# Kernel tuning notes

Measured on AMD Instinct MI355X. Metric: run time of the kernel, lower is better.

## Reference

```python
import jax, jax.numpy as jnp
import numpy as np

NUM_HEADS = 8
GROUPS = 32
EPS = 1e-5


def setup_inputs() -> dict:
    key = jax.random.key(0)
    k1, k2, k3 = jax.random.split(key, 3)
    B, C, H, W = 16, 512, 64, 64
    x = jax.random.normal(k1, (B, C, H, W), dtype=jnp.float32)
    scale = C ** -0.5  # keep qkv/proj outputs well-scaled
    return {
        "x": x,
        "norm_w": jnp.ones((C,), jnp.float32),
        "norm_b": jnp.zeros((C,), jnp.float32),
        "qkv_w": jax.random.normal(k2, (3 * C, C), dtype=jnp.float32) * scale,
        "qkv_b": jnp.zeros((3 * C,), jnp.float32),
        "proj_w": jax.random.normal(k3, (C, C), dtype=jnp.float32) * scale,
        "proj_b": jnp.zeros((C,), jnp.float32),
    }


def reference(x, norm_w, norm_b, qkv_w, qkv_b, proj_w, proj_b):
    B, C, H, W = x.shape
    N = H * W
    nh = NUM_HEADS
    hd = C // nh

    # GroupNorm(32, C)
    xg = x.reshape(B, GROUPS, C // GROUPS, N)
    mu = xg.mean(axis=(2, 3), keepdims=True)
    var = xg.var(axis=(2, 3), keepdims=True)
    h = ((xg - mu) * jax.lax.rsqrt(var + EPS)).reshape(B, C, N)
    h = h * norm_w[None, :, None] + norm_b[None, :, None]

    h = h.transpose(0, 2, 1)  # [B, N, C]
    qkv = (h @ qkv_w.T + qkv_b).reshape(B, N, 3, nh, hd)
    q, k, v = qkv[:, :, 0], qkv[:, :, 1], qkv[:, :, 2]  # each [B, N, nh, hd]

    # Faithful to source: attention over the HEAD axis at each position
    attn = jnp.einsum('bnhd,bngd->bnhg', q, k) * (hd ** -0.5)  # [B, N, nh, nh]
    attn = jax.nn.softmax(attn, axis=-1)
    o = jnp.einsum('bnhg,bngd->bnhd', attn, v).reshape(B, N, C)

    o = o @ proj_w.T + proj_b  # [B, N, C]
    return x + o.transpose(0, 2, 1).reshape(B, C, H, W)
```

## Files before the change

kernel.cpp:

```cpp
#include <hip/hip_runtime.h>

typedef __attribute__((ext_vector_type(8))) short short8v;
typedef __attribute__((ext_vector_type(4))) float float4v;
typedef unsigned short ushortT;

__device__ __forceinline__ unsigned short f2bf(float f) {
  union { float f; unsigned u; } a; a.f = f;
  unsigned r = a.u + 0x7fffu + ((a.u >> 16) & 1u);
  return (unsigned short)(r >> 16);
}
__device__ __forceinline__ float2 up2(unsigned u) {
  union { unsigned u; float f; } a, b;
  a.u = u << 16; b.u = u & 0xffff0000u;
  return make_float2(a.f, b.f);
}
__device__ __forceinline__ void gl_lds16(const void* g, void* l) {
  __builtin_amdgcn_global_load_lds(
      (const __attribute__((address_space(1))) void*)g,
      (__attribute__((address_space(3))) void*)l, 16, 0, 0);
}

#define WAITV4 asm volatile("s_waitcnt vmcnt(4)" ::: "memory")
#define WAITV0 asm volatile("s_waitcnt vmcnt(0)" ::: "memory")
#define BAR()  __builtin_amdgcn_s_barrier()
#define MFMA16(d, a, b) d = __builtin_amdgcn_mfma_f32_16x16x32_bf16(a, b, d, 0, 0, 0)

__global__ __launch_bounds__(256) void prep(const float* __restrict__ qkvw,
                                            const float* __restrict__ pw,
                                            const float* __restrict__ x,
                                            ushortT* __restrict__ wq_b,
                                            ushortT* __restrict__ wp_b,
                                            float2* __restrict__ stats) {
  int bid = blockIdx.x, tid = threadIdx.x;
  if (bid < 1024) {
    const float* src = (bid < 768) ? qkvw : pw;
    ushortT* dst     = (bid < 768) ? wq_b : wp_b;
    int base = (bid < 768) ? bid : (bid - 768);
    int i = (base * 256 + tid) * 4;
    float4 v = *(const float4*)(src + i);
    uint2 o;
    o.x = (unsigned)f2bf(v.x) | ((unsigned)f2bf(v.y) << 16);
    o.y = (unsigned)f2bf(v.z) | ((unsigned)f2bf(v.w) << 16);
    *(uint2*)(dst + i) = o;
    return;
  }
  int bg = bid - 1024;
  const float* base = x + (size_t)bg * 65536;
  float s = 0.f, s2 = 0.f;
  for (int i = tid; i < 16384; i += 256) {
    float4 v = *(const float4*)(base + (size_t)i * 4);
    s  += v.x + v.y + v.z + v.w;
    s2 += v.x * v.x + v.y * v.y + v.z * v.z + v.w * v.w;
  }
  #pragma unroll
  for (int off = 32; off > 0; off >>= 1) {
    s  += __shfl_down(s, off);
    s2 += __shfl_down(s2, off);
  }
  __shared__ float red[8];
  int w = tid >> 6, l = tid & 63;
  if (l == 0) { red[w] = s; red[w + 4] = s2; }
  __syncthreads();
  if (tid == 0) {
    float ts = red[0] + red[1] + red[2] + red[3];
    float t2 = red[4] + red[5] + red[6] + red[7];
    float mean = ts * (1.f / 65536.f);
    float var  = t2 * (1.f / 65536.f) - mean * mean;
    stats[bg] = make_float2(mean, rsqrtf(var + 1e-5f));
  }
}

__global__ __launch_bounds__(512) void norm_tr(const float* __restrict__ x,
                                               const float* __restrict__ nw,
                                               const float* __restrict__ nb,
                                               const float2* __restrict__ stats,
                                               ushortT* __restrict__ h) {
  __shared__ float t[64][65];
  int n0 = blockIdx.x * 64, c0 = blockIdx.y * 64, b = blockIdx.z;
  int tx = threadIdx.x, ty = threadIdx.y;
  #pragma unroll
  for (int j = ty; j < 64; j += 8) {
    int c = c0 + j;
    float2 ms = stats[b * 32 + (c >> 4)];
    float v = x[((size_t)b * 512 + c) * 4096 + n0 + tx];
    t[j][tx] = (v - ms.x) * ms.y * nw[c] + nb[c];
  }
  __syncthreads();
  #pragma unroll
  for (int j = ty; j < 64; j += 8) {
    int n = n0 + j;
    h[((size_t)b * 4096 + n) * 512 + c0 + tx] = f2bf(t[tx][j]);
  }
}

__device__ __forceinline__ void core256b(const ushortT* __restrict__ A,
                                         const ushortT* __restrict__ Bm,
                                         ushortT* lds, int m0, int n0,
                                         float4v (&acc)[8][4]) {
  char* ldsb = (char*)lds;
  const int tid = threadIdx.x;
  const int w = tid >> 6, l = tid & 63;
  const int wm = w >> 2, wn = w & 3;

  const int P0b = tid * 16, P1b = 8192 + tid * 16;
  const int r0 = P0b >> 7, r1 = P1b >> 7;
  const int s0 = (P0b & 127) ^ ((r0 & 7) << 4);
  const int s1 = (P1b & 127) ^ ((r1 & 7) << 4);
  const size_t g0 = (size_t)r0 * 512 + (s0 >> 1);
  const size_t g1 = (size_t)r1 * 512 + (s1 >> 1);
  auto stage = [&](const ushortT* mat, int rowbase, int kt, int bufb, int region) {
    const ushortT* gsrc = mat + (size_t)rowbase * 512 + kt * 64;
    char* dbase = ldsb + bufb + region;
    gl_lds16(gsrc + g0, dbase + P0b);
    gl_lds16(gsrc + g1, dbase + P1b);
  };

  const int colb = (l >> 4) * 16;
  const int cs0 = colb ^ ((l & 7) << 4);
  const int cs1 = (64 + colb) ^ ((l & 7) << 4);
  const int arow = wm * 16384 + (l & 15) * 128;
  const int brow = 32768 + wn * 8192 + (l & 15) * 128;

  short8v Af[4][2], Bf[4][2];

  #define RDA4(bb, MH)                                                  \
    { _Pragma("unroll")                                                 \
      for (int mm = 0; mm < 4; ++mm) {                                  \
        const char* p = ldsb + (bb) + arow + ((MH)*4 + mm) * 2048;      \
        Af[mm][0] = *(const short8v*)(p + cs0);                         \
        Af[mm][1] = *(const short8v*)(p + cs1);                         \
      } }
  #define RDB2(bb, N0)                                                  \
    { _Pragma("unroll")                                                 \
      for (int nn = 0; nn < 2; ++nn) {                                  \
        const char* p = ldsb + (bb) + brow + ((N0) + nn) * 2048;        \
        Bf[(N0)+nn][0] = *(const short8v*)(p + cs0);                    \
        Bf[(N0)+nn][1] = *(const short8v*)(p + cs1);                    \
      } }
  #define CLUSTER(MH, NP)                                               \
    { __builtin_amdgcn_s_setprio(1);                                    \
      _Pragma("unroll")                                                 \
      for (int mm = 0; mm < 4; ++mm) {                                  \
        _Pragma("unroll")                                               \
        for (int nn = 0; nn < 2; ++nn) {                                \
          MFMA16(acc[(MH)*4+mm][(NP)*2+nn], Af[mm][0], Bf[(NP)*2+nn][0]); \
          MFMA16(acc[(MH)*4+mm][(NP)*2+nn], Af[mm][1], Bf[(NP)*2+nn][1]); \
        } }                                                             \
      __builtin_amdgcn_s_setprio(0); }

  auto tile = [&](int bb, int t1, int t2, bool s1g, bool s2g, int vw) {
    RDB2(bb, 0); RDA4(bb, 0);
    if (s1g) stage(A, m0 + 128, t1, bb ^ 65536, 16384);
    BAR();
    CLUSTER(0, 0);
    BAR();
    RDB2(bb, 2);
    if (s1g) stage(Bm, n0 + 128, t1, bb ^ 65536, 49152);
    BAR();
    CLUSTER(0, 1);
    BAR();
    RDA4(bb, 1);
    if (s2g) stage(Bm, n0, t2, bb, 32768);
    BAR();
    CLUSTER(1, 1);
    BAR();
    if (s2g) stage(A, m0, t2, bb, 0);
    if (vw == 4)      { WAITV4; }
    else if (vw == 0) { WAITV0; }
    BAR();
    CLUSTER(1, 0);
    BAR();
  };

  stage(A,  m0,       0, 0, 0);
  stage(A,  m0 + 128, 0, 0, 16384);
  stage(Bm, n0,       0, 0, 32768);
  stage(Bm, n0 + 128, 0, 0, 49152);
  stage(Bm, n0,       1, 65536, 32768);
  stage(A,  m0,       1, 65536, 0);
  WAITV4;
  BAR();

  #pragma unroll 1
  for (int tp = 0; tp < 3; ++tp) {
    tile(0,     2 * tp + 1, 2 * tp + 2, true, true, 4);
    tile(65536, 2 * tp + 2, 2 * tp + 3, true, true, 4);
  }
  tile(0,     7, 8, true,  false, 0);
  tile(65536, 8, 9, false, false, -1);
  #undef RDA4
  #undef RDB2
  #undef CLUSTER
}

__global__ __launch_bounds__(512, 2) void gemm_qkv(const ushortT* __restrict__ h,
                                                   const ushortT* __restrict__ wq,
                                                   const float* __restrict__ bias,
                                                   ushortT* __restrict__ outq) {
  __shared__ ushortT lds[65536];
  int bid = blockIdx.x;
  int wg = (bid & 7) * 192 + (bid >> 3);
  int m0 = (wg / 6) * 256, n0 = (wg % 6) * 256;
  float4v acc[8][4] = {};
  core256b(h, wq, lds, m0, n0, acc);
  const int tid = threadIdx.x;
  const int w = tid >> 6, l = tid & 63;
  const int wm = w >> 2, wn = w & 3;
  __syncthreads();
  ushortT* es = lds + w * 1280;
  float bb[4];
  #pragma unroll
  for (int fn = 0; fn < 4; ++fn) bb[fn] = bias[n0 + wn * 64 + fn * 16 + (l & 15)];
  int r = l >> 2, g = l & 3;
  #pragma unroll
  for (int fm = 0; fm < 8; ++fm) {
    #pragma unroll
    for (int fn = 0; fn < 4; ++fn)
      #pragma unroll
      for (int j = 0; j < 4; ++j)
        es[((l >> 4) * 4 + j) * 72 + fn * 16 + (l & 15)] = f2bf(acc[fm][fn][j] + bb[fn]);
    uint4 v0 = *(const uint4*)(es + r * 72 + g * 16);
    uint4 v1 = *(const uint4*)(es + r * 72 + g * 16 + 8);
    size_t mrow = (size_t)m0 + wm * 128 + fm * 16 + r;
    uint4* dst = (uint4*)(outq + mrow * 1536 + n0 + wn * 64 + g * 16);
    dst[0] = v0; dst[1] = v1;
  }
}

__global__ __launch_bounds__(256) void attn_k(const ushortT* __restrict__ qkv,
                                              ushortT* __restrict__ o) {
  int gp = blockIdx.x * 256 + threadIdx.x;
  int pos = gp >> 3, hh = gp & 7;
  const ushortT* base = qkv + (size_t)pos * 1536;

  float lg[8];
  {
    unsigned qu[32];
    const uint4* qs = (const uint4*)(base + hh * 64);
    #pragma unroll
    for (int i = 0; i < 8; ++i) {
      uint4 u = qs[i];
      qu[i*4+0] = u.x; qu[i*4+1] = u.y; qu[i*4+2] = u.z; qu[i*4+3] = u.w;
    }
    #pragma unroll
    for (int g = 0; g < 8; ++g) {
      float s = 0.f;
      #pragma unroll
      for (int d8 = 0; d8 < 8; ++d8) {
        uint4 kk = *(const uint4*)(base + 512 + g * 64 + d8 * 8);
        float2 k0 = up2(kk.x), k1 = up2(kk.y), k2 = up2(kk.z), k3 = up2(kk.w);
        float2 q0 = up2(qu[d8*4+0]), q1 = up2(qu[d8*4+1]);
        float2 q2 = up2(qu[d8*4+2]), q3 = up2(qu[d8*4+3]);
        s += q0.x*k0.x + q0.y*k0.y + q1.x*k1.x + q1.y*k1.y
           + q2.x*k2.x + q2.y*k2.y + q3.x*k3.x + q3.y*k3.y;
      }
      lg[g] = s * 0.125f;
    }
  }
  float mx = lg[0];
  #pragma unroll
  for (int g = 1; g < 8; ++g) mx = fmaxf(mx, lg[g]);
  float ssum = 0.f;
  #pragma unroll
  for (int g = 0; g < 8; ++g) { lg[g] = __expf(lg[g] - mx); ssum += lg[g]; }
  float inv = 1.f / ssum;
  #pragma unroll
  for (int g = 0; g < 8; ++g) lg[g] *= inv;

  ushortT* dst = o + (size_t)pos * 512 + hh * 64;
  #pragma unroll 1
  for (int half = 0; half < 2; ++half) {
    float oa[32];
    #pragma unroll
    for (int i = 0; i < 32; ++i) oa[i] = 0.f;
    const ushortT* vb = base + 1024 + half * 32;
    #pragma unroll
    for (int g = 0; g < 8; ++g) {
      float wg = lg[g];
      #pragma unroll
      for (int d4 = 0; d4 < 4; ++d4) {
        uint4 vv = *(const uint4*)(vb + g * 64 + d4 * 8);
        float2 v0 = up2(vv.x), v1 = up2(vv.y), v2 = up2(vv.z), v3 = up2(vv.w);
        oa[d4*8+0] += wg*v0.x; oa[d4*8+1] += wg*v0.y;
        oa[d4*8+2] += wg*v1.x; oa[d4*8+3] += wg*v1.y;
        oa[d4*8+4] += wg*v2.x; oa[d4*8+5] += wg*v2.y;
        oa[d4*8+6] += wg*v3.x; oa[d4*8+7] += wg*v3.y;
      }
    }
    #pragma unroll
    for (int i = 0; i < 4; ++i) {
      uint4 w_;
      w_.x = (unsigned)f2bf(oa[i*8+0]) | ((unsigned)f2bf(oa[i*8+1]) << 16);
      w_.y = (unsigned)f2bf(oa[i*8+2]) | ((unsigned)f2bf(oa[i*8+3]) << 16);
      w_.z = (unsigned)f2bf(oa[i*8+4]) | ((unsigned)f2bf(oa[i*8+5]) << 16);
      w_.w = (unsigned)f2bf(oa[i*8+6]) | ((unsigned)f2bf(oa[i*8+7]) << 16);
      *(uint4*)(dst + half * 32 + i * 8) = w_;
    }
  }
}

__global__ __launch_bounds__(512, 2) void gemm_proj(const ushortT* __restrict__ o,
                                                    const ushortT* __restrict__ wp,
                                                    const float* __restrict__ bias,
                                                    const float* __restrict__ x,
                                                    float* __restrict__ out) {
  __shared__ ushortT lds[65536];
  int bid = blockIdx.x;
  int wg = (bid & 7) * 64 + (bid >> 3);
  int m0 = (wg >> 1) * 256, n0 = (wg & 1) * 256;
  float4v acc[8][4] = {};
  core256b(o, wp, lds, m0, n0, acc);
  const int tid = threadIdx.x;
  const int w = tid >> 6, l = tid & 63;
  const int wm = w >> 2, wn = w & 3;
  __syncthreads();
  float* es = (float*)((char*)lds + w * 4608);
  int b = m0 >> 12;
  int c = n0 + wn * 64 + l;
  float bc = bias[c];
  const float* xrow = x + ((size_t)b * 512 + c) * 4096;
  float* orow = out + ((size_t)b * 512 + c) * 4096;
  int nb0 = (m0 & 4095) + wm * 128;
  #pragma unroll
  for (int fm = 0; fm < 8; ++fm) {
    #pragma unroll
    for (int fn = 0; fn < 4; ++fn)
      #pragma unroll
      for (int j = 0; j < 4; ++j)
        es[((l >> 4) * 4 + j) * 68 + fn * 16 + (l & 15)] = acc[fm][fn][j];
    int nb = nb0 + fm * 16;
    #pragma unroll
    for (int q4 = 0; q4 < 4; ++q4) {
      float4 xv = *(const float4*)(xrow + nb + q4 * 4);
      float4 ov;
      ov.x = xv.x + bc + es[(q4 * 4 + 0) * 68 + l];
      ov.y = xv.y + bc + es[(q4 * 4 + 1) * 68 + l];
      ov.z = xv.z + bc + es[(q4 * 4 + 2) * 68 + l];
      ov.w = xv.w + bc + es[(q4 * 4 + 3) * 68 + l];
      *(float4*)(orow + nb + q4 * 4) = ov;
    }
  }
}

extern "C" void kernel_launch(void* const* d_in, const int* in_sizes, int n_in,
                              void* d_out, int out_size, void* d_ws, size_t ws_size,
                              hipStream_t stream) {
  const float* x     = (const float*)d_in[0];
  const float* nw    = (const float*)d_in[1];
  const float* nb    = (const float*)d_in[2];
  const float* qkvw  = (const float*)d_in[3];
  const float* qkvb  = (const float*)d_in[4];
  const float* pw    = (const float*)d_in[5];
  const float* pb    = (const float*)d_in[6];
  float* out = (float*)d_out;
  char* ws = (char*)d_ws;

  const size_t OFF_WQ   = 4096;
  const size_t OFF_WP   = OFF_WQ + 1572864;
  const size_t OFF_H    = OFF_WP + 524288;
  const size_t OFF_QKV  = OFF_H + 67108864;

  float2* stats   = (float2*)ws;
  ushortT* wq_b   = (ushortT*)(ws + OFF_WQ);
  ushortT* wp_b   = (ushortT*)(ws + OFF_WP);
  ushortT* h      = (ushortT*)(ws + OFF_H);
  ushortT* qkv    = (ushortT*)(ws + OFF_QKV);

  prep<<<1536, 256, 0, stream>>>(qkvw, pw, x, wq_b, wp_b, stats);
  norm_tr<<<dim3(64, 8, 16), dim3(64, 8), 0, stream>>>(x, nw, nb, stats, h);
  gemm_qkv<<<1536, 512, 0, stream>>>(h, wq_b, qkvb, qkv);
  attn_k<<<2048, 256, 0, stream>>>(qkv, h);
  gemm_proj<<<512, 512, 0, stream>>>(h, wp_b, pb, x, out);
}
```

Measured before the change: 402.6 us.

## Stage per-position QKV rows in LDS and split head dim across thread pairs

The attention kernel now bulk-loads 16 positions' full QKV rows into shared memory with direct global-to-LDS copies, then computes from LDS. Each head's 64-dim work is split across two threads, with the partial dot products combined by a lane shuffle, and the grid size is doubled. This targets the redundant, uncoalesced global reads of K and V (each read by all 8 head threads) and cuts per-thread register pressure, at the cost of a barrier and LDS usage.

```diff
diff --git a/kernel.cpp b/kernel.cpp
--- a/kernel.cpp
+++ b/kernel.cpp
@@ -229,33 +229,47 @@
 
 __global__ __launch_bounds__(256) void attn_k(const ushortT* __restrict__ qkv,
                                               ushortT* __restrict__ o) {
-  int gp = blockIdx.x * 256 + threadIdx.x;
-  int pos = gp >> 3, hh = gp & 7;
-  const ushortT* base = qkv + (size_t)pos * 1536;
-
+  __shared__ ushortT kv[16 * 1544];
+  const int tid = threadIdx.x;
+  const int p0 = blockIdx.x * 16;
+
+  #pragma unroll
+  for (int j = 0; j < 12; ++j) {
+    int c = j * 256 + tid;
+    int row = c / 192, col = c % 192;
+    gl_lds16(qkv + (size_t)(p0 + row) * 1536 + col * 8,
+             (char*)kv + row * 3088 + col * 16);
+  }
+  __syncthreads();
+
+  const int pos = tid >> 4, h = (tid >> 1) & 7, dh = tid & 1;
+  const ushortT* rowp = kv + pos * 1544;
+
+  unsigned qv[16];
+  {
+    const uint4* qs = (const uint4*)(rowp + h * 64 + dh * 32);
+    #pragma unroll
+    for (int i = 0; i < 4; ++i) {
+      uint4 u = qs[i];
+      qv[i*4+0] = u.x; qv[i*4+1] = u.y; qv[i*4+2] = u.z; qv[i*4+3] = u.w;
+    }
+  }
   float lg[8];
-  {
-    unsigned qu[32];
-    const uint4* qs = (const uint4*)(base + hh * 64);
-    #pragma unroll
-    for (int i = 0; i < 8; ++i) {
-      uint4 u = qs[i];
-      qu[i*4+0] = u.x; qu[i*4+1] = u.y; qu[i*4+2] = u.z; qu[i*4+3] = u.w;
+  #pragma unroll
+  for (int g = 0; g < 8; ++g) {
+    const uint4* ks = (const uint4*)(rowp + 512 + g * 64 + dh * 32);
+    float s = 0.f;
+    #pragma unroll
+    for (int i = 0; i < 4; ++i) {
+      uint4 u = ks[i];
+      float2 k0 = up2(u.x), k1 = up2(u.y), k2 = up2(u.z), k3 = up2(u.w);
+      float2 q0 = up2(qv[i*4+0]), q1 = up2(qv[i*4+1]);
+      float2 q2 = up2(qv[i*4+2]), q3 = up2(qv[i*4+3]);
+      s += q0.x*k0.x + q0.y*k0.y + q1.x*k1.x + q1.y*k1.y
+         + q2.x*k2.x + q2.y*k2.y + q3.x*k3.x + q3.y*k3.y;
     }
-    #pragma unroll
-    for (int g = 0; g < 8; ++g) {
-      float s = 0.f;
-      #pragma unroll
-      for (int d8 = 0; d8 < 8; ++d8) {
-        uint4 kk = *(const uint4*)(base + 512 + g * 64 + d8 * 8);
-        float2 k0 = up2(kk.x), k1 = up2(kk.y), k2 = up2(kk.z), k3 = up2(kk.w);
-        float2 q0 = up2(qu[d8*4+0]), q1 = up2(qu[d8*4+1]);
-        float2 q2 = up2(qu[d8*4+2]), q3 = up2(qu[d8*4+3]);
-        s += q0.x*k0.x + q0.y*k0.y + q1.x*k1.x + q1.y*k1.y
-           + q2.x*k2.x + q2.y*k2.y + q3.x*k3.x + q3.y*k3.y;
-      }
-      lg[g] = s * 0.125f;
-    }
+    s += __shfl_xor(s, 1);
+    lg[g] = s * 0.125f;
   }
   float mx = lg[0];
   #pragma unroll
@@ -267,35 +281,32 @@
   #pragma unroll
   for (int g = 0; g < 8; ++g) lg[g] *= inv;
 
-  ushortT* dst = o + (size_t)pos * 512 + hh * 64;
-  #pragma unroll 1
-  for (int half = 0; half < 2; ++half) {
-    float oa[32];
-    #pragma unroll
-    for (int i = 0; i < 32; ++i) oa[i] = 0.f;
-    const ushortT* vb = base + 1024 + half * 32;
-    #pragma unroll
-    for (int g = 0; g < 8; ++g) {
-      float wg = lg[g];
-      #pragma unroll
-      for (int d4 = 0; d4 < 4; ++d4) {
-        uint4 vv = *(const uint4*)(vb + g * 64 + d4 * 8);
-        float2 v0 = up2(vv.x), v1 = up2(vv.y), v2 = up2(vv.z), v3 = up2(vv.w);
-        oa[d4*8+0] += wg*v0.x; oa[d4*8+1] += wg*v0.y;
-        oa[d4*8+2] += wg*v1.x; oa[d4*8+3] += wg*v1.y;
-        oa[d4*8+4] += wg*v2.x; oa[d4*8+5] += wg*v2.y;
-        oa[d4*8+6] += wg*v3.x; oa[d4*8+7] += wg*v3.y;
-      }
+  float oa[32];
+  #pragma unroll
+  for (int i = 0; i < 32; ++i) oa[i] = 0.f;
+  #pragma unroll
+  for (int g = 0; g < 8; ++g) {
+    const uint4* vs = (const uint4*)(rowp + 1024 + g * 64 + dh * 32);
+    float wg = lg[g];
+    #pragma unroll
+    for (int i = 0; i < 4; ++i) {
+      uint4 u = vs[i];
+      float2 v0 = up2(u.x), v1 = up2(u.y), v2 = up2(u.z), v3 = up2(u.w);
+      oa[i*8+0] += wg*v0.x; oa[i*8+1] += wg*v0.y;
+      oa[i*8+2] += wg*v1.x; oa[i*8+3] += wg*v1.y;
+      oa[i*8+4] += wg*v2.x; oa[i*8+5] += wg*v2.y;
+      oa[i*8+6] += wg*v3.x; oa[i*8+7] += wg*v3.y;
     }
-    #pragma unroll
-    for (int i = 0; i < 4; ++i) {
-      uint4 w_;
-      w_.x = (unsigned)f2bf(oa[i*8+0]) | ((unsigned)f2bf(oa[i*8+1]) << 16);
-      w_.y = (unsigned)f2bf(oa[i*8+2]) | ((unsigned)f2bf(oa[i*8+3]) << 16);
-      w_.z = (unsigned)f2bf(oa[i*8+4]) | ((unsigned)f2bf(oa[i*8+5]) << 16);
-      w_.w = (unsigned)f2bf(oa[i*8+6]) | ((unsigned)f2bf(oa[i*8+7]) << 16);
-      *(uint4*)(dst + half * 32 + i * 8) = w_;
-    }
+  }
+  ushortT* dst = o + (size_t)(p0 + pos) * 512 + h * 64 + dh * 32;
+  #pragma unroll
+  for (int i = 0; i < 4; ++i) {
+    uint4 w_;
+    w_.x = (unsigned)f2bf(oa[i*8+0]) | ((unsigned)f2bf(oa[i*8+1]) << 16);
+    w_.y = (unsigned)f2bf(oa[i*8+2]) | ((unsigned)f2bf(oa[i*8+3]) << 16);
+    w_.z = (unsigned)f2bf(oa[i*8+4]) | ((unsigned)f2bf(oa[i*8+5]) << 16);
+    w_.w = (unsigned)f2bf(oa[i*8+6]) | ((unsigned)f2bf(oa[i*8+7]) << 16);
+    *(uint4*)(dst + i * 8) = w_;
   }
 }
 
@@ -369,6 +380,6 @@
   prep<<<1536, 256, 0, stream>>>(qkvw, pw, x, wq_b, wp_b, stats);
   norm_tr<<<dim3(64, 8, 16), dim3(64, 8), 0, stream>>>(x, nw, nb, stats, h);
   gemm_qkv<<<1536, 512, 0, stream>>>(h, wq_b, qkvb, qkv);
-  attn_k<<<2048, 256, 0, stream>>>(qkv, h);
+  attn_k<<<4096, 256, 0, stream>>>(qkv, h);
   gemm_proj<<<512, 512, 0, stream>>>(h, wp_b, pb, x, out);
 }
```

After: 367.9 us. 8.6% less time.
